# Optimization experiments

Measured on AMD Instinct MI355X. Metric: run time of the kernel, lower is better.

## Reference

```python
import jax, jax.numpy as jnp
import numpy as np

M, N, DIM = 256, 256, 512
N_ITER = 2000
ALPHA = 0.5
SIGMA = max(M, N) / 2.0  # 128.0
EPS = 1e-6  # torch.nn.PairwiseDistance default eps (added to the difference)


def setup_inputs() -> dict:
    key = jax.random.key(0)
    k1, k2 = jax.random.split(key)
    x = jax.random.normal(k1, (DIM,), dtype=jnp.float32)
    weights = jax.random.normal(k2, (M * N, DIM), dtype=jnp.float32)
    ii, jj = jnp.meshgrid(jnp.arange(M), jnp.arange(N), indexing='ij')
    locations = jnp.stack([ii, jj], axis=-1).reshape(M * N, 2).astype(jnp.float32)
    return {"x": x, "weights": weights, "locations": locations, "it": 100}


def reference(x, weights, locations, it):
    # distances from x to every codebook row (PairwiseDistance p=2, eps=1e-6)
    diff = x[None, :] - weights + EPS            # (m*n, dim)
    distances = jnp.sqrt(jnp.sum(diff * diff, axis=1))
    bmu_idx = jnp.argmin(distances)
    bmu_loc = locations[bmu_idx]                 # (2,)

    decay = float(np.exp(-it / N_ITER))          # python-scalar, weak-typed
    rate = ALPHA * decay
    sigma_t = SIGMA * decay

    loc_diff = bmu_loc[None, :] - locations + EPS    # (m*n, 2)
    loc_dist = jnp.sqrt(jnp.sum(loc_diff * loc_diff, axis=1))
    influence = jnp.exp(-(loc_dist ** 2) / (2.0 * sigma_t ** 2))[:, None]  # (m*n, 1)

    new_weights = weights + rate * influence * (x[None, :] - weights)
    return new_weights, bmu_idx
```

## Files before the change

### kernel.cpp

```cpp
#include <hip/hip_runtime.h>

#define MN   (256 * 256)
#define DIM  512
#define NF4  (MN * (DIM / 4))
#define EPS  1e-6f

__global__ __launch_bounds__(256) void som_dist(const float* __restrict__ w,
                                                const float* __restrict__ x,
                                                unsigned long long* __restrict__ best) {
    const int lane = threadIdx.x & 63;
    const int wave = threadIdx.x >> 6;
    const int row0 = (blockIdx.x * 4 + wave) * 16;

    const float4* x4 = (const float4*)x;
    float4 xa = x4[lane * 2 + 0];
    float4 xb = x4[lane * 2 + 1];
    xa.x += EPS; xa.y += EPS; xa.z += EPS; xa.w += EPS;
    xb.x += EPS; xb.y += EPS; xb.z += EPS; xb.w += EPS;

    float bestd = 3.4e38f;
    int   besti = 0;

    #pragma unroll
    for (int rb = 0; rb < 16; rb += 8) {
        float4 wa[8], wb[8];
        #pragma unroll
        for (int j = 0; j < 8; ++j) {
            const float4* w4 = (const float4*)(w + (size_t)(row0 + rb + j) * DIM);
            wa[j] = w4[lane * 2 + 0];
            wb[j] = w4[lane * 2 + 1];
        }

        float s[8];
        #pragma unroll
        for (int j = 0; j < 8; ++j) {
            float d, t;
            d = xa.x - wa[j].x; t  = d * d;
            d = xa.y - wa[j].y; t += d * d;
            d = xa.z - wa[j].z; t += d * d;
            d = xa.w - wa[j].w; t += d * d;
            d = xb.x - wb[j].x; t += d * d;
            d = xb.y - wb[j].y; t += d * d;
            d = xb.z - wb[j].z; t += d * d;
            d = xb.w - wb[j].w; t += d * d;
            s[j] = t;
        }

        #pragma unroll
        for (int off = 1; off < 64; off <<= 1) {
            #pragma unroll
            for (int j = 0; j < 8; ++j)
                s[j] += __shfl_xor(s[j], off, 64);
        }

        #pragma unroll
        for (int j = 0; j < 8; ++j) {
            if (s[j] < bestd) { bestd = s[j]; besti = row0 + rb + j; }
        }
    }

    if (lane == 0) {
        unsigned long long key =
            ((unsigned long long)__float_as_uint(bestd) << 32) |
            (unsigned long long)(unsigned)besti;
        atomicMin(best, key);
    }
}

__global__ __launch_bounds__(256) void som_update(const float* __restrict__ w,
                                                  const float* __restrict__ x,
                                                  float* __restrict__ out,
                                                  const unsigned long long* __restrict__ best,
                                                  const int* __restrict__ itp) {
    const int lane = threadIdx.x & 63;
    const int row  = blockIdx.x * 4 + (threadIdx.x >> 6);

    const unsigned long long key = *best;
    const int bmu = (int)(key & 0xffffffffull);

    const int iv = *itp;
    const float itf = (iv >= 0 && iv <= 2000000) ? (float)iv : __int_as_float(iv);

    const double decayd = exp(-(double)itf / 2000.0);
    const float  rate   = 0.5f * (float)decayd;
    const double sigmat = 128.0 * decayd;
    const float  twoS2  = (float)(2.0 * sigmat * sigmat);

    const float d0 = (float)(bmu >> 8)  - (float)(row >> 8)  + EPS;
    const float d1 = (float)(bmu & 255) - (float)(row & 255) + EPS;
    const float ld = sqrtf(d0 * d0 + d1 * d1);
    const float f  = rate * expf(-(ld * ld) / twoS2);

    const size_t base = (size_t)row * 128 + lane * 2;
    const float4 w0 = ((const float4*)w)[base + 0];
    const float4 w1 = ((const float4*)w)[base + 1];
    const float4 x0 = ((const float4*)x)[lane * 2 + 0];
    const float4 x1 = ((const float4*)x)[lane * 2 + 1];

    float4 o0, o1;
    o0.x = w0.x + f * (x0.x - w0.x);
    o0.y = w0.y + f * (x0.y - w0.y);
    o0.z = w0.z + f * (x0.z - w0.z);
    o0.w = w0.w + f * (x0.w - w0.w);
    o1.x = w1.x + f * (x1.x - w1.x);
    o1.y = w1.y + f * (x1.y - w1.y);
    o1.z = w1.z + f * (x1.z - w1.z);
    o1.w = w1.w + f * (x1.w - w1.w);
    ((float4*)out)[base + 0] = o0;
    ((float4*)out)[base + 1] = o1;

    if (row == 0 && lane == 0) {
        out[(size_t)MN * DIM] = (float)bmu;
    }
}

extern "C" void kernel_launch(void* const* d_in, const int* in_sizes, int n_in,
                              void* d_out, int out_size, void* d_ws, size_t ws_size,
                              hipStream_t stream) {
    const float* x = (const float*)d_in[0];
    const float* w = (const float*)d_in[1];
    const int*   it = (const int*)d_in[3];

    float* out = (float*)d_out;
    unsigned long long* best = (unsigned long long*)d_ws;

    hipMemsetAsync(d_ws, 0xFF, sizeof(unsigned long long), stream);

    som_dist<<<1024, 256, 0, stream>>>(w, x, best);
    som_update<<<MN / 4, 256, 0, stream>>>(w, x, out, best, it);
}
```

Baseline: 279.0 us.

## Spread BMU atomics across slots, reduce per block, nontemporal output stores

The distance kernel now gives each wave 8 rows and runs twice as many blocks, which raises parallelism. Wave minima are combined in shared memory so each block issues one atomicMin, and blocks are spread over 8 padded slots to cut contention on a single address. The update kernel takes the minimum over the slots and writes its output with nontemporal stores so the 128MB result does not pollute cache. The cost is an extra shared-memory sync per block and 8 slot reads per update thread.

```diff
diff --git a/kernel.cpp b/kernel.cpp
--- a/kernel.cpp
+++ b/kernel.cpp
@@ -2,15 +2,19 @@
 
 #define MN   (256 * 256)
 #define DIM  512
-#define NF4  (MN * (DIM / 4))
 #define EPS  1e-6f
+
+#define NSLOT      8
+#define SLOT_STRIDE 16
+
+typedef float vfloat4 __attribute__((ext_vector_type(4)));
 
 __global__ __launch_bounds__(256) void som_dist(const float* __restrict__ w,
                                                 const float* __restrict__ x,
-                                                unsigned long long* __restrict__ best) {
+                                                unsigned long long* __restrict__ slots) {
     const int lane = threadIdx.x & 63;
     const int wave = threadIdx.x >> 6;
-    const int row0 = (blockIdx.x * 4 + wave) * 16;
+    const int row0 = (blockIdx.x * 4 + wave) * 8;
 
     const float4* x4 = (const float4*)x;
     float4 xa = x4[lane * 2 + 0];
@@ -18,65 +22,74 @@
     xa.x += EPS; xa.y += EPS; xa.z += EPS; xa.w += EPS;
     xb.x += EPS; xb.y += EPS; xb.z += EPS; xb.w += EPS;
 
-    float bestd = 3.4e38f;
-    int   besti = 0;
+    const float* p = w + (size_t)row0 * DIM + lane * 8;
+
+    float4 wa[8], wb[8];
+    #pragma unroll
+    for (int j = 0; j < 8; ++j) {
+        wa[j] = ((const float4*)(p + j * DIM))[0];
+        wb[j] = ((const float4*)(p + j * DIM))[1];
+    }
+
+    float s[8];
+    #pragma unroll
+    for (int j = 0; j < 8; ++j) {
+        float d, t;
+        d = xa.x - wa[j].x; t  = d * d;
+        d = xa.y - wa[j].y; t += d * d;
+        d = xa.z - wa[j].z; t += d * d;
+        d = xa.w - wa[j].w; t += d * d;
+        d = xb.x - wb[j].x; t += d * d;
+        d = xb.y - wb[j].y; t += d * d;
+        d = xb.z - wb[j].z; t += d * d;
+        d = xb.w - wb[j].w; t += d * d;
+        s[j] = t;
+    }
 
     #pragma unroll
-    for (int rb = 0; rb < 16; rb += 8) {
-        float4 wa[8], wb[8];
+    for (int off = 1; off < 64; off <<= 1) {
         #pragma unroll
-        for (int j = 0; j < 8; ++j) {
-            const float4* w4 = (const float4*)(w + (size_t)(row0 + rb + j) * DIM);
-            wa[j] = w4[lane * 2 + 0];
-            wb[j] = w4[lane * 2 + 1];
-        }
-
-        float s[8];
-        #pragma unroll
-        for (int j = 0; j < 8; ++j) {
-            float d, t;
-            d = xa.x - wa[j].x; t  = d * d;
-            d = xa.y - wa[j].y; t += d * d;
-            d = xa.z - wa[j].z; t += d * d;
-            d = xa.w - wa[j].w; t += d * d;
-            d = xb.x - wb[j].x; t += d * d;
-            d = xb.y - wb[j].y; t += d * d;
-            d = xb.z - wb[j].z; t += d * d;
-            d = xb.w - wb[j].w; t += d * d;
-            s[j] = t;
-        }
-
-        #pragma unroll
-        for (int off = 1; off < 64; off <<= 1) {
-            #pragma unroll
-            for (int j = 0; j < 8; ++j)
-                s[j] += __shfl_xor(s[j], off, 64);
-        }
-
-        #pragma unroll
-        for (int j = 0; j < 8; ++j) {
-            if (s[j] < bestd) { bestd = s[j]; besti = row0 + rb + j; }
-        }
+        for (int j = 0; j < 8; ++j)
+            s[j] += __shfl_xor(s[j], off, 64);
     }
 
+    float bestd = s[0];
+    int   besti = row0;
+    #pragma unroll
+    for (int j = 1; j < 8; ++j) {
+        if (s[j] < bestd) { bestd = s[j]; besti = row0 + j; }
+    }
+
+    __shared__ unsigned long long wkey[4];
     if (lane == 0) {
-        unsigned long long key =
-            ((unsigned long long)__float_as_uint(bestd) << 32) |
-            (unsigned long long)(unsigned)besti;
-        atomicMin(best, key);
+        wkey[wave] = ((unsigned long long)__float_as_uint(bestd) << 32) |
+                     (unsigned long long)(unsigned)besti;
+    }
+    __syncthreads();
+    if (threadIdx.x == 0) {
+        unsigned long long m = wkey[0];
+        if (wkey[1] < m) m = wkey[1];
+        if (wkey[2] < m) m = wkey[2];
+        if (wkey[3] < m) m = wkey[3];
+        atomicMin(&slots[(blockIdx.x & (NSLOT - 1)) * SLOT_STRIDE], m);
     }
 }
 
 __global__ __launch_bounds__(256) void som_update(const float* __restrict__ w,
                                                   const float* __restrict__ x,
                                                   float* __restrict__ out,
-                                                  const unsigned long long* __restrict__ best,
+                                                  const unsigned long long* __restrict__ slots,
                                                   const int* __restrict__ itp) {
     const int lane = threadIdx.x & 63;
     const int row  = blockIdx.x * 4 + (threadIdx.x >> 6);
 
-    const unsigned long long key = *best;
-    const int bmu = (int)(key & 0xffffffffull);
+    unsigned long long m = slots[0];
+    #pragma unroll
+    for (int i = 1; i < NSLOT; ++i) {
+        unsigned long long v = slots[i * SLOT_STRIDE];
+        if (v < m) m = v;
+    }
+    const int bmu = (int)(m & 0xffffffffull);
 
     const int iv = *itp;
     const float itf = (iv >= 0 && iv <= 2000000) ? (float)iv : __int_as_float(iv);
@@ -97,7 +110,7 @@
     const float4 x0 = ((const float4*)x)[lane * 2 + 0];
     const float4 x1 = ((const float4*)x)[lane * 2 + 1];
 
-    float4 o0, o1;
+    vfloat4 o0, o1;
     o0.x = w0.x + f * (x0.x - w0.x);
     o0.y = w0.y + f * (x0.y - w0.y);
     o0.z = w0.z + f * (x0.z - w0.z);
@@ -106,8 +119,8 @@
     o1.y = w1.y + f * (x1.y - w1.y);
     o1.z = w1.z + f * (x1.z - w1.z);
     o1.w = w1.w + f * (x1.w - w1.w);
-    ((float4*)out)[base + 0] = o0;
-    ((float4*)out)[base + 1] = o1;
+    __builtin_nontemporal_store(o0, (vfloat4*)out + base + 0);
+    __builtin_nontemporal_store(o1, (vfloat4*)out + base + 1);
 
     if (row == 0 && lane == 0) {
         out[(size_t)MN * DIM] = (float)bmu;
@@ -122,10 +135,10 @@
     const int*   it = (const int*)d_in[3];
 
     float* out = (float*)d_out;
-    unsigned long long* best = (unsigned long long*)d_ws;
+    unsigned long long* slots = (unsigned long long*)d_ws;
 
-    hipMemsetAsync(d_ws, 0xFF, sizeof(unsigned long long), stream);
+    (void)hipMemsetAsync(d_ws, 0xFF, NSLOT * SLOT_STRIDE * sizeof(unsigned long long), stream);
 
-    som_dist<<<1024, 256, 0, stream>>>(w, x, best);
-    som_update<<<MN / 4, 256, 0, stream>>>(w, x, out, best, it);
+    som_dist<<<2048, 256, 0, stream>>>(w, x, slots);
+    som_update<<<MN / 4, 256, 0, stream>>>(w, x, out, slots, it);
 }
```

Measured after the change: 268.7 us. 3.7% less time.
